# Kernel tuning notes

Hardware: AMD Instinct MI355X
Metric: run time of the kernel (lower is better)

Reference implementation:

```python
import jax, jax.numpy as jnp
import numpy as np

B, H, S, D = 2, 16, 2048, 128

def setup_inputs() -> dict:
    key = jax.random.key(0)
    kq, kk, kv = jax.random.split(key, 3)
    Q = jax.random.normal(kq, (B, H, S, D), dtype=jnp.float32)
    K = jax.random.normal(kk, (B, H, S, D), dtype=jnp.float32)
    V = jax.random.normal(kv, (B, H, S, D), dtype=jnp.float32)
    return {"Q": Q, "K": K, "V": V}

def reference(Q, K, V):
    # FlashAttentionV3 forward: scaled dot-product attention with causal mask,
    # scale defaults to 1/sqrt(head_dim), dropout=0.
    head_dim = Q.shape[-1]
    scale = 1.0 / jnp.sqrt(jnp.asarray(head_dim, dtype=Q.dtype))
    # scores: [B, H, S, S]
    scores = jnp.einsum('bhqd,bhkd->bhqk', Q, K) * scale
    seq_q, seq_k = Q.shape[2], K.shape[2]
    causal_mask = jnp.tril(jnp.ones((seq_q, seq_k), dtype=bool))  # [S, S]
    scores = jnp.where(causal_mask, scores, jnp.asarray(-jnp.inf, dtype=scores.dtype))
    attn = jax.nn.softmax(scores, axis=-1)
    out = jnp.einsum('bhqk,bhkd->bhqd', attn, V)
    return out
```

## Files before the change

kernel.cpp:

```cpp
#include <hip/hip_runtime.h>
#include <hip/hip_bf16.h>

typedef __attribute__((ext_vector_type(8))) short short8;
typedef __attribute__((ext_vector_type(4))) float f32x4;
typedef __attribute__((ext_vector_type(4))) unsigned int u32x4;

#define S_LEN 2048
#define D_DIM 128
#define NT 32
#define NQT 32
#define TILE_FRAG_BYTES 16384u
#define VF_OFF ((size_t)32 * NT * TILE_FRAG_BYTES)

__device__ __forceinline__ unsigned short bfbits(float f) {
  return __builtin_bit_cast(unsigned short, __float2bfloat16(f));
}
__device__ __forceinline__ unsigned int pk2(float lo, float hi) {
  return (unsigned int)bfbits(lo) | ((unsigned int)bfbits(hi) << 16);
}
__device__ __forceinline__ float exp2f_hw(float x) {
  float r;
  asm("v_exp_f32 %0, %1" : "=v"(r) : "v"(x));
  return r;
}
__device__ __forceinline__ void gload16(const void* g, void* l) {
  __builtin_amdgcn_global_load_lds(
      (const __attribute__((address_space(1))) unsigned int*)g,
      (__attribute__((address_space(3))) unsigned int*)l, 16, 0, 0);
}

extern "C" __global__ void __launch_bounds__(256)
fa_prepass_kernel(const float* __restrict__ Kg, const float* __restrict__ Vg,
                  char* __restrict__ ws)
{
  const unsigned gid = blockIdx.x * 256 + threadIdx.x;
  const unsigned g = gid & ((1u << 20) - 1);
  const int ln = g & 63, l15 = ln & 15, lhi = (ln >> 4) & 3;
  const int f  = (g >> 6) & 15;
  const int t  = (g >> 10) & 31;
  const int bh = g >> 15;
  char* dst = ws + ((size_t)(bh * NT + t) * 16 + f) * 1024 + ln * 16;
  if (gid < (1u << 20)) {
    const int c = f >> 2, kk = f & 3;
    const int row = t * 64 + ((l15 >> 2) << 3) + (l15 & 3) + ((c & 1) << 2) + ((c >> 1) << 5);
    const float* src = Kg + (size_t)bh * S_LEN * D_DIM + (size_t)row * D_DIM + kk * 32 + lhi * 8;
    f32x4 a = *(const f32x4*)src;
    f32x4 b = *(const f32x4*)(src + 4);
    u32x4 u;
    u[0] = pk2(a[0], a[1]); u[1] = pk2(a[2], a[3]);
    u[2] = pk2(b[0], b[1]); u[3] = pk2(b[2], b[3]);
    *(u32x4*)dst = u;
  } else {
    const int dc = f >> 1, w = f & 1;
    const float* src = Vg + (size_t)bh * S_LEN * D_DIM
                     + (size_t)(t * 64 + w * 32 + lhi * 8) * D_DIM + dc * 16 + l15;
    float v[8];
    #pragma unroll
    for (int j = 0; j < 8; ++j) v[j] = src[(size_t)j * D_DIM];
    u32x4 u;
    u[0] = pk2(v[0], v[1]); u[1] = pk2(v[2], v[3]);
    u[2] = pk2(v[4], v[5]); u[3] = pk2(v[6], v[7]);
    *(u32x4*)(dst + VF_OFF) = u;
  }
}

extern "C" __global__ void __launch_bounds__(128, 2)
fa_fwd_kernel(const float* __restrict__ Qg, const char* __restrict__ ws,
              float* __restrict__ Og)
{
  __shared__ __align__(16) char smem[2][16384];

  const int bh = blockIdx.x;
  const int by = (int)blockIdx.y;
  int qt;
  if      (by <  8) qt = 31 - by;
  else if (by < 16) qt = by - 8;
  else if (by < 24) qt = 39 - by;
  else              qt = by - 16;
  const int tid = threadIdx.x;
  const int wv  = tid >> 6;
  const int ln  = tid & 63;
  const int l15 = ln & 15;
  const int lhi = ln >> 4;

  const float* Qb = Qg + (size_t)bh * S_LEN * D_DIM;
  float*       Ob = Og + (size_t)bh * S_LEN * D_DIM;
  const char*  kfb = ws + (size_t)bh * NT * TILE_FRAG_BYTES;
  const char*  vfbg = kfb + VF_OFF;
  const int    voff = ln * 16;

  const float scale = 0.12753102f;
  const int wrow_lo = qt * 64 + wv * 32;

  short8 qf[2][4];
  #pragma unroll
  for (int g = 0; g < 2; ++g) {
    const float* qsrc = Qb + (size_t)(wrow_lo + g * 16 + l15) * D_DIM + lhi * 8;
    #pragma unroll
    for (int kk = 0; kk < 4; ++kk) {
      f32x4 a = *(const f32x4*)(qsrc + kk * 32);
      f32x4 b = *(const f32x4*)(qsrc + kk * 32 + 4);
      u32x4 u;
      u[0] = pk2(a[0] * scale, a[1] * scale);
      u[1] = pk2(a[2] * scale, a[3] * scale);
      u[2] = pk2(b[0] * scale, b[1] * scale);
      u[3] = pk2(b[2] * scale, b[3] * scale);
      qf[g][kk] = __builtin_bit_cast(short8, u);
    }
  }

  auto stage_k = [&](int t, char* buf) {
    const char* kt = kfb + (size_t)t * TILE_FRAG_BYTES;
    #pragma unroll
    for (int i = 0; i < 8; ++i) {
      const int fi = wv * 8 + i;
      gload16(kt + (size_t)fi * 1024 + voff, buf + fi * 1024);
    }
  };

  const f32x4 fzero = {0.f, 0.f, 0.f, 0.f};
  f32x4 oacc[2][8];
  #pragma unroll
  for (int g = 0; g < 2; ++g)
    #pragma unroll
    for (int i = 0; i < 8; ++i) oacc[g][i] = fzero;
  float m_run[2] = {8.0f, 8.0f};
  float l_part[2] = {0.f, 0.f};
  float mtp[2];

  short8 vf[16];
  short8 pf[2][2];

  const int ntiles = qt + 1;

  stage_k(0, smem[0]);
  __syncthreads();

  int cur = 0;
  for (int t = 0; t < ntiles; ++t) {
    if (t + 1 < ntiles) stage_k(t + 1, smem[cur ^ 1]);

    const char* kt = smem[cur];
    f32x4 sacc[2][4];
    __builtin_amdgcn_s_setprio(1);
    #pragma unroll
    for (int c = 0; c < 4; ++c) {
      sacc[0][c] = fzero; sacc[1][c] = fzero;
      #pragma unroll
      for (int kk = 0; kk < 4; ++kk) {
        short8 kf = *(const short8*)(kt + (c * 4 + kk) * 1024 + voff);
        sacc[0][c] = __builtin_amdgcn_mfma_f32_16x16x32_bf16(kf, qf[0][kk], sacc[0][c], 0, 0, 0);
        sacc[1][c] = __builtin_amdgcn_mfma_f32_16x16x32_bf16(kf, qf[1][kk], sacc[1][c], 0, 0, 0);
      }
    }
    __builtin_amdgcn_s_setprio(0);

    if (t > 0) {
      __builtin_amdgcn_s_setprio(1);
      #pragma unroll
      for (int dc = 0; dc < 8; ++dc)
        #pragma unroll
        for (int w = 0; w < 2; ++w) {
          oacc[0][dc] = __builtin_amdgcn_mfma_f32_16x16x32_bf16(vf[dc * 2 + w], pf[0][w], oacc[0][dc], 0, 0, 0);
          oacc[1][dc] = __builtin_amdgcn_mfma_f32_16x16x32_bf16(vf[dc * 2 + w], pf[1][w], oacc[1][dc], 0, 0, 0);
        }
      __builtin_amdgcn_s_setprio(0);

      #pragma unroll
      for (int g = 0; g < 2; ++g) {
        if (!__all(mtp[g] <= m_run[g] + 11.5f)) {
          float m = fmaxf(mtp[g], __shfl_xor(mtp[g], 16));
          m = fmaxf(m, __shfl_xor(m, 32));
          const float m_new = fmaxf(m_run[g], m);
          const float al = exp2f_hw(m_run[g] - m_new);
          #pragma unroll
          for (int dc = 0; dc < 8; ++dc)
            #pragma unroll
            for (int r = 0; r < 4; ++r) oacc[g][dc][r] *= al;
          l_part[g] *= al;
          m_run[g] = m_new;
        }
      }
    }

    const char* vg = vfbg + (size_t)t * TILE_FRAG_BYTES;
    #pragma unroll
    for (int i = 0; i < 16; ++i)
      vf[i] = *(const short8*)(vg + i * 1024 + voff);

    if (t == ntiles - 1) {
      #pragma unroll
      for (int g = 0; g < 2; ++g) {
        const int qg = wrow_lo + g * 16 + l15;
        #pragma unroll
        for (int c = 0; c < 4; ++c) {
          const int kvb = t * 64 + (c >> 1) * 32 + (c & 1) * 4 + lhi * 8;
          #pragma unroll
          for (int r = 0; r < 4; ++r)
            if (kvb + r > qg) sacc[g][c][r] = -INFINITY;
        }
      }
    }

    #pragma unroll
    for (int g = 0; g < 2; ++g) {
      float mA[4];
      #pragma unroll
      for (int r = 0; r < 4; ++r)
        mA[r] = fmaxf(fmaxf(sacc[g][0][r], sacc[g][1][r]),
                      fmaxf(sacc[g][2][r], sacc[g][3][r]));
      mtp[g] = fmaxf(fmaxf(mA[0], mA[1]), fmaxf(mA[2], mA[3]));

      #pragma unroll
      for (int c = 0; c < 4; ++c)
        #pragma unroll
        for (int r = 0; r < 4; ++r)
          sacc[g][c][r] = exp2f_hw(sacc[g][c][r] - m_run[g]);

      float sA[4];
      #pragma unroll
      for (int r = 0; r < 4; ++r)
        sA[r] = (sacc[g][0][r] + sacc[g][1][r]) + (sacc[g][2][r] + sacc[g][3][r]);
      l_part[g] += (sA[0] + sA[1]) + (sA[2] + sA[3]);

      #pragma unroll
      for (int w = 0; w < 2; ++w) {
        u32x4 u;
        u[0] = pk2(sacc[g][2 * w][0], sacc[g][2 * w][1]);
        u[1] = pk2(sacc[g][2 * w][2], sacc[g][2 * w][3]);
        u[2] = pk2(sacc[g][2 * w + 1][0], sacc[g][2 * w + 1][1]);
        u[3] = pk2(sacc[g][2 * w + 1][2], sacc[g][2 * w + 1][3]);
        pf[g][w] = __builtin_bit_cast(short8, u);
      }
    }

    __syncthreads();
    cur ^= 1;
  }

  __builtin_amdgcn_s_setprio(1);
  #pragma unroll
  for (int dc = 0; dc < 8; ++dc)
    #pragma unroll
    for (int w = 0; w < 2; ++w) {
      oacc[0][dc] = __builtin_amdgcn_mfma_f32_16x16x32_bf16(vf[dc * 2 + w], pf[0][w], oacc[0][dc], 0, 0, 0);
      oacc[1][dc] = __builtin_amdgcn_mfma_f32_16x16x32_bf16(vf[dc * 2 + w], pf[1][w], oacc[1][dc], 0, 0, 0);
    }
  __builtin_amdgcn_s_setprio(0);

  #pragma unroll
  for (int g = 0; g < 2; ++g) {
    float l = l_part[g];
    l += __shfl_xor(l, 16);
    l += __shfl_xor(l, 32);
    const float invl = 1.0f / l;
    float* orow = Ob + (size_t)(wrow_lo + g * 16 + l15) * D_DIM + lhi * 4;
    #pragma unroll
    for (int dc = 0; dc < 8; ++dc) {
      f32x4 o;
      #pragma unroll
      for (int r = 0; r < 4; ++r) o[r] = oacc[g][dc][r] * invl;
      *(f32x4*)(orow + dc * 16) = o;
    }
  }
}

extern "C" void kernel_launch(void* const* d_in, const int* in_sizes, int n_in,
                              void* d_out, int out_size, void* d_ws, size_t ws_size,
                              hipStream_t stream) {
  const float* Q = (const float*)d_in[0];
  const float* K = (const float*)d_in[1];
  const float* V = (const float*)d_in[2];
  float* O = (float*)d_out;
  char* ws = (char*)d_ws;
  fa_prepass_kernel<<<dim3(8192), dim3(256), 0, stream>>>(K, V, ws);
  dim3 grid(32 , NQT);
  fa_fwd_kernel<<<grid, dim3(128), 0, stream>>>(Q, ws, O);
}
```

Measured before the change: 81.49 us.

## Split long causal query tiles across two blocks with a merge kernel

```diff
diff --git a/kernel.cpp b/kernel.cpp
--- a/kernel.cpp
+++ b/kernel.cpp
@@ -4,13 +4,17 @@
 typedef __attribute__((ext_vector_type(8))) short short8;
 typedef __attribute__((ext_vector_type(4))) float f32x4;
 typedef __attribute__((ext_vector_type(4))) unsigned int u32x4;
+typedef __attribute__((ext_vector_type(2))) unsigned int u32x2;
 
 #define S_LEN 2048
 #define D_DIM 128
 #define NT 32
-#define NQT 32
 #define TILE_FRAG_BYTES 16384u
 #define VF_OFF ((size_t)32 * NT * TILE_FRAG_BYTES)
+#define FRAG_WS 33554432ull
+#define PO_OFF  FRAG_WS
+#define PML_OFF (FRAG_WS + 17825792ull)
+#define WS_NEED (FRAG_WS + 17825792ull + 557056ull)
 
 __device__ __forceinline__ unsigned short bfbits(float f) {
   return __builtin_bit_cast(unsigned short, __float2bfloat16(f));
@@ -65,18 +69,35 @@
 }
 
 extern "C" __global__ void __launch_bounds__(128, 2)
-fa_fwd_kernel(const float* __restrict__ Qg, const char* __restrict__ ws,
-              float* __restrict__ Og)
+fa_fwd_kernel(const float* __restrict__ Qg, char* __restrict__ ws,
+              float* __restrict__ Og, int split_on)
 {
   __shared__ __align__(16) char smem[2][16384];
 
   const int bh = blockIdx.x;
   const int by = (int)blockIdx.y;
-  int qt;
-  if      (by <  8) qt = 31 - by;
-  else if (by < 16) qt = by - 8;
-  else if (by < 24) qt = 39 - by;
-  else              qt = by - 16;
+  int qt, s = 0, t0, t1;
+  bool has_partial = false;
+  if (split_on) {
+    if (by < 34) {
+      qt = 31 - (by >> 1);
+      s  = by & 1;
+      const int nt = qt + 1, h = (nt + 1) >> 1;
+      t0 = s ? h : 0;
+      t1 = s ? nt : h;
+      has_partial = true;
+    } else {
+      qt = 48 - by;
+      t0 = 0; t1 = qt + 1;
+    }
+  } else {
+    if      (by <  8) qt = 31 - by;
+    else if (by < 16) qt = by - 8;
+    else if (by < 24) qt = 39 - by;
+    else              qt = by - 16;
+    t0 = 0; t1 = qt + 1;
+  }
+
   const int tid = threadIdx.x;
   const int wv  = tid >> 6;
   const int ln  = tid & 63;
@@ -131,14 +152,12 @@
   short8 vf[16];
   short8 pf[2][2];
 
-  const int ntiles = qt + 1;
-
-  stage_k(0, smem[0]);
+  stage_k(t0, smem[0]);
   __syncthreads();
 
   int cur = 0;
-  for (int t = 0; t < ntiles; ++t) {
-    if (t + 1 < ntiles) stage_k(t + 1, smem[cur ^ 1]);
+  for (int t = t0; t < t1; ++t) {
+    if (t + 1 < t1) stage_k(t + 1, smem[cur ^ 1]);
 
     const char* kt = smem[cur];
     f32x4 sacc[2][4];
@@ -155,7 +174,7 @@
     }
     __builtin_amdgcn_s_setprio(0);
 
-    if (t > 0) {
+    if (t > t0) {
       __builtin_amdgcn_s_setprio(1);
       #pragma unroll
       for (int dc = 0; dc < 8; ++dc)
@@ -188,7 +207,7 @@
     for (int i = 0; i < 16; ++i)
       vf[i] = *(const short8*)(vg + i * 1024 + voff);
 
-    if (t == ntiles - 1) {
+    if (t == qt) {
       #pragma unroll
       for (int g = 0; g < 2; ++g) {
         const int qg = wrow_lo + g * 16 + l15;
@@ -248,20 +267,74 @@
     }
   __builtin_amdgcn_s_setprio(0);
 
+  if (!has_partial) {
+    #pragma unroll
+    for (int g = 0; g < 2; ++g) {
+      float l = l_part[g];
+      l += __shfl_xor(l, 16);
+      l += __shfl_xor(l, 32);
+      const float invl = 1.0f / l;
+      float* orow = Ob + (size_t)(wrow_lo + g * 16 + l15) * D_DIM + lhi * 4;
+      #pragma unroll
+      for (int dc = 0; dc < 8; ++dc) {
+        f32x4 o;
+        #pragma unroll
+        for (int r = 0; r < 4; ++r) o[r] = oacc[g][dc][r] * invl;
+        *(f32x4*)(orow + dc * 16) = o;
+      }
+    }
+  } else {
+    const int slot = (bh * 17 + (qt - 15)) * 2 + s;
+    char*  pO  = ws + PO_OFF + (size_t)slot * 64 * 128 * 2;
+    float* pML = (float*)(ws + PML_OFF) + (size_t)slot * 64 * 2;
+    #pragma unroll
+    for (int g = 0; g < 2; ++g) {
+      float l = l_part[g];
+      l += __shfl_xor(l, 16);
+      l += __shfl_xor(l, 32);
+      const int row = wv * 32 + g * 16 + l15;
+      #pragma unroll
+      for (int dc = 0; dc < 8; ++dc) {
+        u32x2 w2;
+        w2[0] = pk2(oacc[g][dc][0], oacc[g][dc][1]);
+        w2[1] = pk2(oacc[g][dc][2], oacc[g][dc][3]);
+        *(u32x2*)(pO + (row * 128 + dc * 16 + lhi * 4) * 2) = w2;
+      }
+      if (lhi == 0) {
+        pML[row * 2]     = m_run[g];
+        pML[row * 2 + 1] = l;
+      }
+    }
+  }
+}
+
+extern "C" __global__ void __launch_bounds__(256)
+fa_merge_kernel(const char* __restrict__ ws, float* __restrict__ Og)
+{
+  const int bh = blockIdx.x, qtl = blockIdx.y;
+  const int slotA = (bh * 17 + qtl) * 2, slotB = slotA + 1;
+  const __hip_bfloat16* pOA = (const __hip_bfloat16*)(ws + PO_OFF) + (size_t)slotA * 8192;
+  const __hip_bfloat16* pOB = (const __hip_bfloat16*)(ws + PO_OFF) + (size_t)slotB * 8192;
+  const float* mlA = (const float*)(ws + PML_OFF) + (size_t)slotA * 128;
+  const float* mlB = (const float*)(ws + PML_OFF) + (size_t)slotB * 128;
+  float* Ob = Og + ((size_t)bh * S_LEN + (size_t)(15 + qtl) * 64) * D_DIM;
+
   #pragma unroll
-  for (int g = 0; g < 2; ++g) {
-    float l = l_part[g];
-    l += __shfl_xor(l, 16);
-    l += __shfl_xor(l, 32);
-    const float invl = 1.0f / l;
-    float* orow = Ob + (size_t)(wrow_lo + g * 16 + l15) * D_DIM + lhi * 4;
-    #pragma unroll
-    for (int dc = 0; dc < 8; ++dc) {
-      f32x4 o;
-      #pragma unroll
-      for (int r = 0; r < 4; ++r) o[r] = oacc[g][dc][r] * invl;
-      *(f32x4*)(orow + dc * 16) = o;
-    }
+  for (int it = 0; it < 8; ++it) {
+    const int wi = it * 256 + threadIdx.x;
+    const int row = wi >> 5;
+    const int d4  = (wi & 31) * 4;
+    const float mA = mlA[row * 2], lA = mlA[row * 2 + 1];
+    const float mB = mlB[row * 2], lB = mlB[row * 2 + 1];
+    const float ms = fmaxf(mA, mB);
+    const float wA = exp2f(mA - ms), wB = exp2f(mB - ms);
+    const float inv = 1.0f / (lA * wA + lB * wB);
+    f32x4 o;
+    #pragma unroll
+    for (int j = 0; j < 4; ++j)
+      o[j] = (__bfloat162float(pOA[row * 128 + d4 + j]) * wA +
+              __bfloat162float(pOB[row * 128 + d4 + j]) * wB) * inv;
+    *(f32x4*)(Ob + (size_t)row * D_DIM + d4) = o;
   }
 }
 
@@ -273,7 +346,10 @@
   const float* V = (const float*)d_in[2];
   float* O = (float*)d_out;
   char* ws = (char*)d_ws;
+  const int split_on = (ws_size >= WS_NEED) ? 1 : 0;
   fa_prepass_kernel<<<dim3(8192), dim3(256), 0, stream>>>(K, V, ws);
-  dim3 grid(32 , NQT);
-  fa_fwd_kernel<<<grid, dim3(128), 0, stream>>>(Q, ws, O);
-}
+  dim3 grid(32, split_on ? 49 : 32);
+  fa_fwd_kernel<<<grid, dim3(128), 0, stream>>>(Q, ws, O, split_on);
+  if (split_on)
+    fa_merge_kernel<<<dim3(32, 17), dim3(256), 0, stream>>>(ws, O);
+}
```

Measured after the change: 92.76 us. 1.14x slower.
